# Kernel tuning notes

Hardware: AMD Instinct MI355X
Metric: run time of the kernel (lower is better)

Reference implementation:

```python
import jax, jax.numpy as jnp
import numpy as np

BN_EPS = 1e-5


def setup_inputs() -> dict:
    key = jax.random.key(0)
    k_h, k_e, k_w, k_b = jax.random.split(key, 4)
    B, N, d = 8, 256, 128
    h = jax.random.normal(k_h, (B, N, d), dtype=jnp.float32)
    e = jax.random.normal(k_e, (B, N, N, d), dtype=jnp.float32)
    # Linear(d, d) params (PyTorch default init: U(-1/sqrt(d), 1/sqrt(d)))
    lim = 1.0 / np.sqrt(d)
    W = jax.random.uniform(k_w, (d, d), minval=-lim, maxval=lim, dtype=jnp.float32)
    b = jax.random.uniform(k_b, (d,), minval=-lim, maxval=lim, dtype=jnp.float32)
    # BatchNorm1d affine params (default init: gamma=1, beta=0)
    gamma = jnp.ones((d,), dtype=jnp.float32)
    beta = jnp.zeros((d,), dtype=jnp.float32)
    return {"h": h, "e": e, "W": W, "b": b, "gamma": gamma, "beta": beta}


def reference(h, e, W, b, gamma, beta):
    B, N, d = h.shape
    # Edge scalar weight: L2 norm over feature dim -> (B, N, N)
    w = jnp.linalg.norm(e, axis=-1)
    # Softmax over source-node axis (dim=2)
    w = jax.nn.softmax(w, axis=2)
    # Weighted aggregation of neighbor features: (B, N, d)
    agg = jnp.einsum('bij,bjd->bid', w, h)
    # Linear + ReLU
    h_new = jax.nn.relu(jnp.einsum('bnd,kd->bnk', h + agg, W) + b)
    # BatchNorm1d over flattened (B*N, d), training-mode batch statistics
    x = h_new.reshape(B * N, d)
    mean = jnp.mean(x, axis=0)
    var = jnp.var(x, axis=0)  # biased variance, as torch BN uses for normalization
    x = (x - mean) * jax.lax.rsqrt(var + BN_EPS) * gamma + beta
    h_new = x.reshape(B, N, d) + h
    return (h_new, e)
```

## Files before the change

kernel.cpp:

```cpp
#include <hip/hip_runtime.h>

#define BB 8
#define NN 256
#define DD 128
#define NROWS ((long)BB * NN * NN)
#define NBI   (BB * NN)

__global__ __launch_bounds__(256) void k_norm_copy(const float4* __restrict__ e,
                                                   float4* __restrict__ eo,
                                                   float* __restrict__ w) {
    const int tid  = threadIdx.x;
    const int q    = tid & 31;
    const int rsub = tid >> 5;
    for (long base = (long)blockIdx.x * 8; base < NROWS; base += (long)gridDim.x * 8) {
        const long r   = base + rsub;
        const long idx = r * 32 + q;
        float4 v = e[idx];
        eo[idx] = v;
        float s = v.x * v.x + v.y * v.y + v.z * v.z + v.w * v.w;
        #pragma unroll
        for (int m = 16; m >= 1; m >>= 1) s += __shfl_xor(s, m, 64);
        if (q == 0) w[r] = sqrtf(s);
    }
}

__global__ __launch_bounds__(256) void k_softmax_agg(const float* __restrict__ w,
                                                     const float* __restrict__ h,
                                                     float* __restrict__ x) {
    const int bi  = blockIdx.x;
    const int b   = bi >> 8;
    const int tid = threadIdx.x;
    __shared__ float p[NN];
    __shared__ float red[8];
    __shared__ float acc2[DD];

    float v = w[(long)bi * NN + tid];
    float m = v;
    #pragma unroll
    for (int msk = 32; msk >= 1; msk >>= 1) m = fmaxf(m, __shfl_xor(m, msk, 64));
    const int wid = tid >> 6, lane = tid & 63;
    if (lane == 0) red[wid] = m;
    __syncthreads();
    m = fmaxf(fmaxf(red[0], red[1]), fmaxf(red[2], red[3]));
    float ev = __expf(v - m);
    float s = ev;
    #pragma unroll
    for (int msk = 32; msk >= 1; msk >>= 1) s += __shfl_xor(s, msk, 64);
    if (lane == 0) red[4 + wid] = s;
    __syncthreads();
    s = (red[4] + red[5]) + (red[6] + red[7]);
    p[tid] = ev / s;
    __syncthreads();

    const int d  = tid & 127;
    const int j0 = (tid >> 7) << 7;
    const float* hb = h + ((long)b * NN + j0) * DD + d;
    float acc = 0.f;
    #pragma unroll 8
    for (int j = 0; j < 128; ++j) acc += p[j0 + j] * hb[(long)j * DD];
    if (tid >= 128) acc2[d] = acc;
    __syncthreads();
    if (tid < 128) {
        const long o = (long)bi * DD + d;
        x[o] = h[o] + acc + acc2[d];
    }
}

__global__ __launch_bounds__(128) void k_linear(const float* __restrict__ x,
                                                const float* __restrict__ W,
                                                const float* __restrict__ bias,
                                                float* __restrict__ y) {
    const int row = blockIdx.x;
    const int k   = threadIdx.x;
    __shared__ float xs[DD];
    xs[k] = x[(long)row * DD + k];
    __syncthreads();
    const float* wr = W + (long)k * DD;
    float acc = bias[k];
    #pragma unroll 4
    for (int d = 0; d < DD; ++d) acc += xs[d] * wr[d];
    acc = fmaxf(acc, 0.f);
    y[(long)row * DD + k] = acc;
}

__global__ __launch_bounds__(256) void k_stats(const float* __restrict__ y,
                                               float* __restrict__ sums) {
    const int k = blockIdx.x;
    const int t = threadIdx.x;
    float s = 0.f, s2 = 0.f;
    for (int r = t; r < NBI; r += 256) {
        float v = y[(long)r * DD + k];
        s += v; s2 += v * v;
    }
    __shared__ float ls[256], ls2[256];
    ls[t] = s; ls2[t] = s2;
    __syncthreads();
    for (int off = 128; off >= 1; off >>= 1) {
        if (t < off) { ls[t] += ls[t + off]; ls2[t] += ls2[t + off]; }
        __syncthreads();
    }
    if (t == 0) { sums[k] = ls[0]; sums[DD + k] = ls2[0]; }
}

__global__ __launch_bounds__(256) void k_bn(const float* __restrict__ y,
                                            const float* __restrict__ h,
                                            const float* __restrict__ sums,
                                            const float* __restrict__ gamma,
                                            const float* __restrict__ beta,
                                            float* __restrict__ out) {
    const long i = (long)blockIdx.x * blockDim.x + threadIdx.x;
    if (i >= (long)NBI * DD) return;
    const int k = (int)(i & (DD - 1));
    const float inv_n = 1.f / (float)NBI;
    float mean = sums[k] * inv_n;
    float var  = sums[DD + k] * inv_n - mean * mean;
    float inv  = rsqrtf(var + 1e-5f);
    out[i] = (y[i] - mean) * inv * gamma[k] + beta[k] + h[i];
}

extern "C" void kernel_launch(void* const* d_in, const int* in_sizes, int n_in,
                              void* d_out, int out_size, void* d_ws, size_t ws_size,
                              hipStream_t stream) {
    const float* h     = (const float*)d_in[0];
    const float* e     = (const float*)d_in[1];
    const float* W     = (const float*)d_in[2];
    const float* bias  = (const float*)d_in[3];
    const float* gamma = (const float*)d_in[4];
    const float* beta  = (const float*)d_in[5];

    float* out_h = (float*)d_out;
    float* out_e = out_h + (long)NBI * DD;

    float* ws   = (float*)d_ws;
    float* w    = ws;
    float* x    = ws + 524288;
    float* y    = ws + 786432;
    float* sums = ws + 1048576;

    k_norm_copy  <<<2048, 256, 0, stream>>>((const float4*)e, (float4*)out_e, w);
    k_softmax_agg<<<NBI,  256, 0, stream>>>(w, h, x);
    k_linear     <<<NBI,  128, 0, stream>>>(x, W, bias, y);
    k_stats      <<<DD,   256, 0, stream>>>(y, sums);
    k_bn         <<<(NBI * DD + 255) / 256, 256, 0, stream>>>(y, h, sums, gamma, beta, out_h);
}
```

Baseline: 489.1 us.

## Fuse edge-norm copy, softmax aggregation and linear into one per-row kernel

Merges the edge norm/copy pass, the softmax aggregation and the linear+ReLU into one kernel with one block per (b,i) row. Each block streams its 256×128 edge slab with nontemporal loads and stores and keeps the norms in shared memory, so the w and x intermediates never go through global memory. W is pre-transposed so the linear reads are coalesced. BatchNorm statistics become a two-level reduction over 64 blocks, and the apply pass is vectorised with a precomputed scale and shift. The cost is more serial work per block and fewer global passes to spread the memory-bound copy across.

```diff
diff --git a/kernel.cpp b/kernel.cpp
--- a/kernel.cpp
+++ b/kernel.cpp
@@ -3,42 +3,59 @@
 #define BB 8
 #define NN 256
 #define DD 128
-#define NROWS ((long)BB * NN * NN)
 #define NBI   (BB * NN)
 
-__global__ __launch_bounds__(256) void k_norm_copy(const float4* __restrict__ e,
-                                                   float4* __restrict__ eo,
-                                                   float* __restrict__ w) {
-    const int tid  = threadIdx.x;
-    const int q    = tid & 31;
-    const int rsub = tid >> 5;
-    for (long base = (long)blockIdx.x * 8; base < NROWS; base += (long)gridDim.x * 8) {
-        const long r   = base + rsub;
-        const long idx = r * 32 + q;
-        float4 v = e[idx];
-        eo[idx] = v;
+typedef float f32x4 __attribute__((ext_vector_type(4)));
+
+#define WS_Y     0
+#define WS_WT    262144
+#define WS_P1    278528
+#define WS_P2    286720
+#define WS_SCALE 294912
+#define WS_SHIFT 295040
+
+__global__ __launch_bounds__(256) void k_transpose(const float* __restrict__ W,
+                                                   float* __restrict__ Wt) {
+    for (int idx = threadIdx.x + blockIdx.x * 256; idx < DD * DD; idx += 256 * 8) {
+        const int k = idx >> 7, d = idx & 127;
+        Wt[d * DD + k] = W[idx];
+    }
+}
+
+__global__ __launch_bounds__(256) void k_fused(const f32x4* __restrict__ e,
+                                               f32x4* __restrict__ eo,
+                                               const float* __restrict__ h,
+                                               const float* __restrict__ Wt,
+                                               const float* __restrict__ bias,
+                                               float* __restrict__ y) {
+    const int bi  = blockIdx.x;
+    const int b   = bi >> 8;
+    const int tid = threadIdx.x;
+
+    __shared__ float sw[NN];
+    __shared__ float red[8];
+    __shared__ float xs[DD];
+    __shared__ float acc2[DD];
+
+    const long slab = (long)bi * 8192;
+    const int  q    = tid & 31;
+    #pragma unroll 4
+    for (int it = 0; it < 32; ++it) {
+        const int f = it * 256 + tid;
+        f32x4 v = __builtin_nontemporal_load(&e[slab + f]);
+        __builtin_nontemporal_store(v, &eo[slab + f]);
         float s = v.x * v.x + v.y * v.y + v.z * v.z + v.w * v.w;
         #pragma unroll
         for (int m = 16; m >= 1; m >>= 1) s += __shfl_xor(s, m, 64);
-        if (q == 0) w[r] = sqrtf(s);
+        if (q == 0) sw[f >> 5] = s;
     }
-}
+    __syncthreads();
 
-__global__ __launch_bounds__(256) void k_softmax_agg(const float* __restrict__ w,
-                                                     const float* __restrict__ h,
-                                                     float* __restrict__ x) {
-    const int bi  = blockIdx.x;
-    const int b   = bi >> 8;
-    const int tid = threadIdx.x;
-    __shared__ float p[NN];
-    __shared__ float red[8];
-    __shared__ float acc2[DD];
-
-    float v = w[(long)bi * NN + tid];
+    const int wid = tid >> 6, lane = tid & 63;
+    float v = sqrtf(sw[tid]);
     float m = v;
     #pragma unroll
     for (int msk = 32; msk >= 1; msk >>= 1) m = fmaxf(m, __shfl_xor(m, msk, 64));
-    const int wid = tid >> 6, lane = tid & 63;
     if (lane == 0) red[wid] = m;
     __syncthreads();
     m = fmaxf(fmaxf(red[0], red[1]), fmaxf(red[2], red[3]));
@@ -49,7 +66,7 @@
     if (lane == 0) red[4 + wid] = s;
     __syncthreads();
     s = (red[4] + red[5]) + (red[6] + red[7]);
-    p[tid] = ev / s;
+    sw[tid] = ev / s;
     __syncthreads();
 
     const int d  = tid & 127;
@@ -57,65 +74,82 @@
     const float* hb = h + ((long)b * NN + j0) * DD + d;
     float acc = 0.f;
     #pragma unroll 8
-    for (int j = 0; j < 128; ++j) acc += p[j0 + j] * hb[(long)j * DD];
+    for (int j = 0; j < 128; ++j) acc += sw[j0 + j] * hb[(long)j * DD];
     if (tid >= 128) acc2[d] = acc;
     __syncthreads();
     if (tid < 128) {
-        const long o = (long)bi * DD + d;
-        x[o] = h[o] + acc + acc2[d];
+        xs[d] = h[(long)bi * DD + d] + acc + acc2[d];
+    }
+    __syncthreads();
+
+    const int k  = tid & 127;
+    const int d0 = (tid >> 7) << 6;
+    float la = 0.f;
+    #pragma unroll 8
+    for (int dd = 0; dd < 64; ++dd) {
+        const int di = d0 + dd;
+        la += xs[di] * Wt[di * DD + k];
+    }
+    if (tid >= 128) acc2[k] = la;
+    __syncthreads();
+    if (tid < 128) {
+        float yv = fmaxf(la + acc2[k] + bias[k], 0.f);
+        y[(long)bi * DD + k] = yv;
     }
 }
 
-__global__ __launch_bounds__(128) void k_linear(const float* __restrict__ x,
-                                                const float* __restrict__ W,
-                                                const float* __restrict__ bias,
-                                                float* __restrict__ y) {
-    const int row = blockIdx.x;
-    const int k   = threadIdx.x;
-    __shared__ float xs[DD];
-    xs[k] = x[(long)row * DD + k];
+__global__ __launch_bounds__(256) void k_stats_a(const float* __restrict__ y,
+                                                 float* __restrict__ p1,
+                                                 float* __restrict__ p2) {
+    const int d  = threadIdx.x & 127;
+    const int rh = threadIdx.x >> 7;
+    const int r0 = blockIdx.x * 32;
+    float s = 0.f, s2 = 0.f;
+    #pragma unroll 4
+    for (int rr = rh; rr < 32; rr += 2) {
+        float vv = y[(long)(r0 + rr) * DD + d];
+        s += vv; s2 += vv * vv;
+    }
+    __shared__ float ls[256], ls2[256];
+    ls[threadIdx.x] = s; ls2[threadIdx.x] = s2;
     __syncthreads();
-    const float* wr = W + (long)k * DD;
-    float acc = bias[k];
-    #pragma unroll 4
-    for (int d = 0; d < DD; ++d) acc += xs[d] * wr[d];
-    acc = fmaxf(acc, 0.f);
-    y[(long)row * DD + k] = acc;
+    if (threadIdx.x < 128) {
+        p1[blockIdx.x * DD + d] = ls[d] + ls[d + 128];
+        p2[blockIdx.x * DD + d] = ls2[d] + ls2[d + 128];
+    }
 }
 
-__global__ __launch_bounds__(256) void k_stats(const float* __restrict__ y,
-                                               float* __restrict__ sums) {
-    const int k = blockIdx.x;
-    const int t = threadIdx.x;
+__global__ __launch_bounds__(128) void k_stats_b(const float* __restrict__ p1,
+                                                 const float* __restrict__ p2,
+                                                 const float* __restrict__ gamma,
+                                                 const float* __restrict__ beta,
+                                                 float* __restrict__ scale,
+                                                 float* __restrict__ shift) {
+    const int d = threadIdx.x;
     float s = 0.f, s2 = 0.f;
-    for (int r = t; r < NBI; r += 256) {
-        float v = y[(long)r * DD + k];
-        s += v; s2 += v * v;
+    #pragma unroll 8
+    for (int bb = 0; bb < 64; ++bb) {
+        s  += p1[bb * DD + d];
+        s2 += p2[bb * DD + d];
     }
-    __shared__ float ls[256], ls2[256];
-    ls[t] = s; ls2[t] = s2;
-    __syncthreads();
-    for (int off = 128; off >= 1; off >>= 1) {
-        if (t < off) { ls[t] += ls[t + off]; ls2[t] += ls2[t + off]; }
-        __syncthreads();
-    }
-    if (t == 0) { sums[k] = ls[0]; sums[DD + k] = ls2[0]; }
+    const float inv_n = 1.f / (float)NBI;
+    float mean = s * inv_n;
+    float var  = s2 * inv_n - mean * mean;
+    float inv  = rsqrtf(var + 1e-5f);
+    float sc   = gamma[d] * inv;
+    scale[d] = sc;
+    shift[d] = beta[d] - mean * sc;
 }
 
-__global__ __launch_bounds__(256) void k_bn(const float* __restrict__ y,
-                                            const float* __restrict__ h,
-                                            const float* __restrict__ sums,
-                                            const float* __restrict__ gamma,
-                                            const float* __restrict__ beta,
-                                            float* __restrict__ out) {
-    const long i = (long)blockIdx.x * blockDim.x + threadIdx.x;
-    if (i >= (long)NBI * DD) return;
-    const int k = (int)(i & (DD - 1));
-    const float inv_n = 1.f / (float)NBI;
-    float mean = sums[k] * inv_n;
-    float var  = sums[DD + k] * inv_n - mean * mean;
-    float inv  = rsqrtf(var + 1e-5f);
-    out[i] = (y[i] - mean) * inv * gamma[k] + beta[k] + h[i];
+__global__ __launch_bounds__(256) void k_apply(const f32x4* __restrict__ y,
+                                               const f32x4* __restrict__ h,
+                                               const f32x4* __restrict__ scale,
+                                               const f32x4* __restrict__ shift,
+                                               f32x4* __restrict__ out) {
+    const int i = blockIdx.x * 256 + threadIdx.x;
+    const int c = i & 31;
+    f32x4 yv = y[i], hv = h[i], sc = scale[c], sh = shift[c];
+    out[i] = yv * sc + sh + hv;
 }
 
 extern "C" void kernel_launch(void* const* d_in, const int* in_sizes, int n_in,
@@ -131,15 +165,20 @@
     float* out_h = (float*)d_out;
     float* out_e = out_h + (long)NBI * DD;
 
-    float* ws   = (float*)d_ws;
-    float* w    = ws;
-    float* x    = ws + 524288;
-    float* y    = ws + 786432;
-    float* sums = ws + 1048576;
+    float* ws    = (float*)d_ws;
+    float* y     = ws + WS_Y;
+    float* Wt    = ws + WS_WT;
+    float* p1    = ws + WS_P1;
+    float* p2    = ws + WS_P2;
+    float* scale = ws + WS_SCALE;
+    float* shift = ws + WS_SHIFT;
 
-    k_norm_copy  <<<2048, 256, 0, stream>>>((const float4*)e, (float4*)out_e, w);
-    k_softmax_agg<<<NBI,  256, 0, stream>>>(w, h, x);
-    k_linear     <<<NBI,  128, 0, stream>>>(x, W, bias, y);
-    k_stats      <<<DD,   256, 0, stream>>>(y, sums);
-    k_bn         <<<(NBI * DD + 255) / 256, 256, 0, stream>>>(y, h, sums, gamma, beta, out_h);
+    k_transpose<<<8,    256, 0, stream>>>(W, Wt);
+    k_fused    <<<NBI,  256, 0, stream>>>((const f32x4*)e, (f32x4*)out_e, h,
+                                          Wt, bias, y);
+    k_stats_a  <<<64,   256, 0, stream>>>(y, p1, p2);
+    k_stats_b  <<<1,    128, 0, stream>>>(p1, p2, gamma, beta, scale, shift);
+    k_apply    <<<256,  256, 0, stream>>>((const f32x4*)y, (const f32x4*)h,
+                                          (const f32x4*)scale, (const f32x4*)shift,
+                                          (f32x4*)out_h);
 }
```

Measured after the change: 469.1 us. -4.1%, faster.
